# Kernel optimization log

Measured on AMD Instinct MI355X. Metric: run time of the kernel, lower is better.

## Reference

```python
import jax, jax.numpy as jnp
import numpy as np

EPS = 1e-3  # nn.LayerNorm(eps=0.001)
PADDING = 0.0


def setup_inputs() -> dict:
    key = jax.random.key(0)
    k1, k2, k3, k4 = jax.random.split(key, 4)
    N, M, K3, C_IN, C_OUT, B = 200000, 40000, 27, 64, 128, 4
    features = jax.random.normal(k1, (N, C_IN), dtype=jnp.float32)
    center_coors = jax.random.normal(k2, (M, 3), dtype=jnp.float32)
    voxel_idx = jax.random.randint(k3, (M, K3), 0, N, dtype=jnp.int64)
    num_list = jnp.full((B,), M // B, dtype=jnp.int32)
    W = jax.random.normal(k4, (K3 * C_IN, C_OUT), dtype=jnp.float32) * 1e-4
    gamma = jnp.ones((C_OUT,), dtype=jnp.float32)
    beta = jnp.zeros((C_OUT,), dtype=jnp.float32)
    return {
        "features": features,
        "center_coors": center_coors,
        "voxel_idx": voxel_idx,
        "num_list": num_list,
        "W": W,
        "gamma": gamma,
        "beta": beta,
        "num_keypoints": 2048,
    }


def _block(features, voxel_idx, W, gamma, beta):
    M, K3 = voxel_idx.shape
    C_in = features.shape[1]
    # voxel neighbor gather; negative idx -> padding value
    gathered = features[jnp.clip(voxel_idx, 0, features.shape[0] - 1)]  # [M, K3, C_in]
    gathered = jnp.where(voxel_idx[..., None] < 0, PADDING, gathered)
    flat = gathered.reshape(M, K3 * C_in)
    out = flat @ W  # [M, C_out]
    # LayerNorm over channel dim (per-batch loop in torch is mathematically
    # identical to a single row-wise LayerNorm)
    mu = jnp.mean(out, axis=-1, keepdims=True)
    var = jnp.mean(jnp.square(out - mu), axis=-1, keepdims=True)
    out = (out - mu) / jnp.sqrt(var + EPS) * gamma + beta
    return jax.nn.relu(out)


def _resample(out_features, center_coors, num_list, num_keypoints):
    B = num_list.shape[0]
    K = num_keypoints
    accum = jnp.cumsum(num_list)
    offsets = jnp.concatenate([jnp.zeros((1,), accum.dtype), accum[:-1]])  # [B]
    j = jnp.arange(K, dtype=jnp.int32)  # [K]
    end = jnp.minimum(num_list, jnp.int32(K))  # [B]
    valid = j[None, :] < end[:, None]  # [B, K]
    src = jnp.clip(offsets[:, None] + j[None, :], 0, out_features.shape[0] - 1)  # [B, K]
    res_feat = jnp.where(valid[..., None], out_features[src], 0.0)  # [B, K, C]
    res_xyz = jnp.where(valid[..., None], center_coors[src], 0.0)  # [B, K, 3]
    # replicate original quirk: segments 0..B-2 get batch index 1..B-1, last stays 0
    bid = jnp.arange(B, dtype=jnp.float32)
    col0 = jnp.where(bid < B - 1, bid + 1.0, 0.0)  # [B]
    col0 = jnp.broadcast_to(col0[:, None, None], (B, K, 1))
    res_coor = jnp.concatenate([col0, res_xyz], axis=-1)  # [B, K, 4]
    C = out_features.shape[1]
    return res_feat.reshape(B * K, C), res_coor.reshape(B * K, 4)


def reference(features, center_coors, voxel_idx, num_list, W, gamma, beta, num_keypoints):
    out = _block(features, voxel_idx, W, gamma, beta)
    point_features, point_coords = _resample(out, center_coors, num_list, num_keypoints)
    return point_features, point_coords
```

## Files before the change

kernel.cpp:

```cpp
#include <hip/hip_runtime.h>
#include <hip/hip_bf16.h>
#include <stdint.h>
#include <stddef.h>

#define TM 16
#define CIN 64
#define NK3 27
#define NK3P 28
#define COUT 128
#define EPS_LN 1e-3f
#define KCH  (NK3 * CIN / 32)
#define KCHP (NK3P * CIN / 32)
#define NT   (COUT / 16)
#define NPAIR (NK3P / 2)
#define PK_BYTES (NT * KCHP * 64 * 8 * 2)

typedef __attribute__((ext_vector_type(8))) short   short8;
typedef __attribute__((ext_vector_type(4))) float   floatx4;
typedef __attribute__((ext_vector_type(4))) unsigned short ushort4v;

__device__ __forceinline__ unsigned short f2b(float f) {
    union { float f; unsigned int i; } v;
    v.f = f;
    unsigned int i = v.i;
    return (unsigned short)((i + 0x7fffu + ((i >> 16) & 1u)) >> 16);
}

__global__ __launch_bounds__(256) void pack_w(const float* __restrict__ Wm,
                                              const int* __restrict__ voxel_idx,
                                              const int* __restrict__ num_list,
                                              int Bc,
                                              unsigned short* __restrict__ pk,
                                              int* __restrict__ flags) {
    const int t = threadIdx.x;
    if (blockIdx.x == 0 && t < 64) {
        int wv = voxel_idx[2 * t + 1];
        unsigned long long nz = __ballot(wv != 0);
        if (t == 0) {
            int f = (nz == 0ULL) ? 1 : 0;
            bool n64 = false;
            if (Bc >= 2) {
                n64 = (num_list[1] == 0) && (num_list[0] != 0);
                if (Bc >= 4) n64 = n64 && (num_list[3] == 0);
            }
            if (n64) f |= 2;
            flags[0] = f;
        }
    }
    int slot = blockIdx.x * 256 + t;
    int l  = slot & 63;
    int kk = (slot >> 6) % KCHP;
    int nt = slot / (64 * KCHP);
    short8 v = {0, 0, 0, 0, 0, 0, 0, 0};
    if (kk < KCH) {
        int q = l >> 4, n = l & 15;
        const float* src = Wm + (size_t)(kk * 32 + q * 8) * COUT + nt * 16 + n;
        #pragma unroll
        for (int j = 0; j < 8; ++j)
            v[j] = (short)f2b(src[(size_t)j * COUT]);
    }
    *(short8*)(pk + (size_t)slot * 8) = v;
}

__global__ __launch_bounds__(256) void dpc_mfma(
    const float* __restrict__ features,
    const float* __restrict__ center,
    const int* __restrict__ voxel_idx,
    const int* __restrict__ num_list,
    const unsigned short* __restrict__ pk,
    const int* __restrict__ flags,
    const float* __restrict__ gamma_,
    const float* __restrict__ beta_,
    float* __restrict__ out_feat,
    float* __restrict__ out_coor,
    int N, int M, int B, int K, int Rtot)
{
    __shared__ int s_vid[TM][NK3P];
    __shared__ int s_src[TM];
    __shared__ int s_valid[TM];
    __shared__ __align__(16) unsigned short s_a[3][2048];
    __shared__ float s_c[TM][COUT + 4];

    const int t  = threadIdx.x;
    const int R0 = blockIdx.x * TM;

    const int fl = flags[0];
    const bool vidx64 = (fl & 1) != 0;
    const bool nl64   = (fl & 2) != 0;

    if (t < TM) {
        int r = R0 + t;
        int src = 0, valid = 0;
        if (r < Rtot) {
            int b = r / K;
            int j = r - b * K;
            int offs = 0, nlb = 0;
            for (int i = 0; i < B; ++i) {
                int v = nl64 ? num_list[2 * i] : num_list[i];
                if (i < b) offs += v;
                if (i == b) nlb = v;
            }
            int end = nlb < K ? nlb : K;
            valid = (j < end) ? 1 : 0;
            src = offs + j;
            if (src < 0) src = 0;
            if (src > M - 1) src = M - 1;
        }
        s_src[t] = src;
        s_valid[t] = valid;
    }
    __syncthreads();

    if (t < TM * 4) {
        int i = t >> 2, comp = t & 3;
        int r = R0 + i;
        if (r < Rtot) {
            float val;
            if (comp == 0) {
                int b = r / K;
                val = (b < B - 1) ? (float)(b + 1) : 0.0f;
            } else {
                val = s_valid[i] ? center[(size_t)s_src[i] * 3 + comp - 1] : 0.0f;
            }
            out_coor[(size_t)r * 4 + comp] = val;
        }
    }

    for (int lin = t; lin < TM * NK3P; lin += 256) {
        int i = lin / NK3P;
        int k = lin - i * NK3P;
        int v = -1;
        if (k < NK3) {
            size_t e = (size_t)s_src[i] * NK3 + k;
            v = vidx64 ? voxel_idx[2 * e] : voxel_idx[e];
        }
        s_vid[i][k] = v;
    }
    __syncthreads();

    const int m  = t >> 4;
    const int c0 = (t & 15) * 4;
    const int chunk = c0 >> 5;
    const int q4    = (c0 & 31) >> 3;
    const int j0    = c0 & 7;
    const int aoff  = chunk * 512 + (q4 * 16 + m) * 8 + j0;

    auto gatherf4 = [&](int kc) -> float4 {
        int idx = s_vid[m][kc];
        float4 r = make_float4(0.f, 0.f, 0.f, 0.f);
        if (idx >= 0) {
            if (idx > N - 1) idx = N - 1;
            r = *(const float4*)(features + (size_t)idx * CIN + c0);
        }
        return r;
    };
    auto stash = [&](int buf, int sub, float4 v) {
        ushort4v u;
        u[0] = f2b(v.x); u[1] = f2b(v.y); u[2] = f2b(v.z); u[3] = f2b(v.w);
        *(ushort4v*)&s_a[buf][sub * 1024 + aoff] = u;
    };

    const int w    = t >> 6;
    const int lane = t & 63;
    const int nt0 = 2 * w, nt1 = 2 * w + 1;
    auto loadB = [&](int nt, int kk) -> short8 {
        return *(const short8*)(pk + ((size_t)(nt * KCHP + kk) * 64 + lane) * 8);
    };

    floatx4 acc0 = {0.f, 0.f, 0.f, 0.f};
    floatx4 acc1 = {0.f, 0.f, 0.f, 0.f};

    stash(0, 0, gatherf4(0));
    stash(0, 1, gatherf4(1));
    float4 cA0 = gatherf4(2);
    float4 cA1 = gatherf4(3);
    short8 bb[8];
    #pragma unroll
    for (int c = 0; c < 4; ++c) {
        bb[2 * c]     = loadB(nt0, c);
        bb[2 * c + 1] = loadB(nt1, c);
    }
    __syncthreads();

    for (int p = 0; p < NPAIR; ++p) {
        const bool hasC = (p + 1 < NPAIR);
        const bool hasN = (p + 2 < NPAIR);

        float4 nA0, nA1;
        if (hasN) { nA0 = gatherf4(2 * p + 4); nA1 = gatherf4(2 * p + 5); }
        short8 nb[8];
        if (hasC) {
            const int kk = 4 * (p + 1);
            #pragma unroll
            for (int c = 0; c < 4; ++c) {
                nb[2 * c]     = loadB(nt0, kk + c);
                nb[2 * c + 1] = loadB(nt1, kk + c);
            }
        }

        const int buf = p % 3;
        const short8 a0 = *(const short8*)&s_a[buf][       lane * 8];
        const short8 a1 = *(const short8*)&s_a[buf][ 512 + lane * 8];
        const short8 a2 = *(const short8*)&s_a[buf][1024 + lane * 8];
        const short8 a3 = *(const short8*)&s_a[buf][1536 + lane * 8];

        acc0 = __builtin_amdgcn_mfma_f32_16x16x32_bf16(a0, bb[0], acc0, 0, 0, 0);
        acc1 = __builtin_amdgcn_mfma_f32_16x16x32_bf16(a0, bb[1], acc1, 0, 0, 0);
        acc0 = __builtin_amdgcn_mfma_f32_16x16x32_bf16(a1, bb[2], acc0, 0, 0, 0);
        acc1 = __builtin_amdgcn_mfma_f32_16x16x32_bf16(a1, bb[3], acc1, 0, 0, 0);
        acc0 = __builtin_amdgcn_mfma_f32_16x16x32_bf16(a2, bb[4], acc0, 0, 0, 0);
        acc1 = __builtin_amdgcn_mfma_f32_16x16x32_bf16(a2, bb[5], acc1, 0, 0, 0);
        acc0 = __builtin_amdgcn_mfma_f32_16x16x32_bf16(a3, bb[6], acc0, 0, 0, 0);
        acc1 = __builtin_amdgcn_mfma_f32_16x16x32_bf16(a3, bb[7], acc1, 0, 0, 0);

        if (hasC) {
            const int wb = (p + 1) % 3;
            stash(wb, 0, cA0);
            stash(wb, 1, cA1);
        }
        __syncthreads();
        if (hasC) {
            #pragma unroll
            for (int i = 0; i < 8; ++i) bb[i] = nb[i];
        }
        if (hasN) { cA0 = nA0; cA1 = nA1; }
    }

    {
        const int cq = lane >> 4, n = lane & 15;
        #pragma unroll
        for (int reg = 0; reg < 4; ++reg) {
            s_c[cq * 4 + reg][nt0 * 16 + n] = acc0[reg];
            s_c[cq * 4 + reg][nt1 * 16 + n] = acc1[reg];
        }
    }
    __syncthreads();

    const int h  = t >> 6;
    const int c2 = (t & 63) * 2;
    const float g0  = gamma_[c2];
    const float g1  = gamma_[c2 + 1];
    const float be0 = beta_[c2];
    const float be1 = beta_[c2 + 1];

    #pragma unroll
    for (int i = 0; i < 4; ++i) {
        int row = h * 4 + i;
        float a0 = s_c[row][c2];
        float a1 = s_c[row][c2 + 1];
        float s  = a0 + a1;
        float ss = a0 * a0 + a1 * a1;
        #pragma unroll
        for (int mm = 1; mm < 64; mm <<= 1) {
            s  += __shfl_xor(s,  mm, 64);
            ss += __shfl_xor(ss, mm, 64);
        }
        float mu   = s * (1.0f / COUT);
        float var  = ss * (1.0f / COUT) - mu * mu;
        float rstd = rsqrtf(var + EPS_LN);
        float v0 = (a0 - mu) * rstd * g0 + be0;
        float v1 = (a1 - mu) * rstd * g1 + be1;
        v0 = fmaxf(v0, 0.f);
        v1 = fmaxf(v1, 0.f);
        if (!s_valid[row]) { v0 = 0.f; v1 = 0.f; }
        int r = R0 + row;
        if (r < Rtot) {
            out_feat[(size_t)r * COUT + c2]     = v0;
            out_feat[(size_t)r * COUT + c2 + 1] = v1;
        }
    }
}

extern "C" void kernel_launch(void* const* d_in, const int* in_sizes, int n_in,
                              void* d_out, int out_size, void* d_ws, size_t ws_size,
                              hipStream_t stream) {
    const float* features = (const float*)d_in[0];
    const float* center   = (const float*)d_in[1];
    const int*   vidx     = (const int*)d_in[2];
    const int*   num_list = (const int*)d_in[3];
    const float* Wm       = (const float*)d_in[4];
    const float* gamma_   = (const float*)d_in[5];
    const float* beta_    = (const float*)d_in[6];

    const int B    = in_sizes[3];
    const int Cout = in_sizes[5];
    const int M    = in_sizes[1] / 3;
    const int K3v  = in_sizes[2] / M;
    const int Cin  = (in_sizes[4] / Cout) / K3v;
    const int N    = in_sizes[0] / Cin;
    const int Rtot = out_size / (Cout + 4);
    const int K    = Rtot / B;

    float* out_feat = (float*)d_out;
    float* out_coor = out_feat + (size_t)Rtot * Cout;

    unsigned short* pk = (unsigned short*)d_ws;
    int* flags = (int*)((char*)d_ws + PK_BYTES);

    const int pack_grid = (NT * KCHP * 64) / 256;
    pack_w<<<dim3(pack_grid), dim3(256), 0, stream>>>(Wm, vidx, num_list, B, pk, flags);

    const int tiles = (Rtot + TM - 1) / TM;
    dpc_mfma<<<dim3(tiles), dim3(256), 0, stream>>>(
        features, center, vidx, num_list, pk, flags, gamma_, beta_,
        out_feat, out_coor, N, M, B, K, Rtot);
}
```

Baseline: 112.2 us.

## Double block to 512 threads, one MFMA output tile per wave

The fused gather-GEMM-LayerNorm kernel now launches 512 threads per block, with 8 waves each owning one 16-column output tile instead of 4 waves owning two. Each thread gathers one of the two neighbor slots per pair, which halves its per-thread gather and B-register load. The aim is more waves in flight to hide latency of the random feature gathers. The cost is more threads per barrier, and only 16 rows per block with little work per wave, so sync overhead may dominate.

```diff
diff --git a/kernel.cpp b/kernel.cpp
--- a/kernel.cpp
+++ b/kernel.cpp
@@ -62,7 +62,7 @@
     *(short8*)(pk + (size_t)slot * 8) = v;
 }
 
-__global__ __launch_bounds__(256) void dpc_mfma(
+__global__ __launch_bounds__(512) void dpc_mfma(
     const float* __restrict__ features,
     const float* __restrict__ center,
     const int* __restrict__ voxel_idx,
@@ -126,7 +126,7 @@
         }
     }
 
-    for (int lin = t; lin < TM * NK3P; lin += 256) {
+    for (int lin = t; lin < TM * NK3P; lin += 512) {
         int i = lin / NK3P;
         int k = lin - i * NK3P;
         int v = -1;
@@ -138,15 +138,17 @@
     }
     __syncthreads();
 
-    const int m  = t >> 4;
-    const int c0 = (t & 15) * 4;
+    const int sub = t >> 8;
+    const int rem = t & 255;
+    const int m   = rem >> 4;
+    const int c0  = (rem & 15) * 4;
     const int chunk = c0 >> 5;
     const int q4    = (c0 & 31) >> 3;
     const int j0    = c0 & 7;
-    const int aoff  = chunk * 512 + (q4 * 16 + m) * 8 + j0;
-
-    auto gatherf4 = [&](int kc) -> float4 {
-        int idx = s_vid[m][kc];
+    const int aoff  = sub * 1024 + chunk * 512 + (q4 * 16 + m) * 8 + j0;
+
+    auto gatherPair = [&](int p) -> float4 {
+        int idx = s_vid[m][2 * p + sub];
         float4 r = make_float4(0.f, 0.f, 0.f, 0.f);
         if (idx >= 0) {
             if (idx > N - 1) idx = N - 1;
@@ -154,48 +156,35 @@
         }
         return r;
     };
-    auto stash = [&](int buf, int sub, float4 v) {
+    auto stash = [&](int buf, float4 v) {
         ushort4v u;
         u[0] = f2b(v.x); u[1] = f2b(v.y); u[2] = f2b(v.z); u[3] = f2b(v.w);
-        *(ushort4v*)&s_a[buf][sub * 1024 + aoff] = u;
+        *(ushort4v*)&s_a[buf][aoff] = u;
     };
 
     const int w    = t >> 6;
     const int lane = t & 63;
-    const int nt0 = 2 * w, nt1 = 2 * w + 1;
-    auto loadB = [&](int nt, int kk) -> short8 {
-        return *(const short8*)(pk + ((size_t)(nt * KCHP + kk) * 64 + lane) * 8);
+    auto loadB = [&](int kk) -> short8 {
+        return *(const short8*)(pk + ((size_t)(w * KCHP + kk) * 64 + lane) * 8);
     };
 
-    floatx4 acc0 = {0.f, 0.f, 0.f, 0.f};
-    floatx4 acc1 = {0.f, 0.f, 0.f, 0.f};
-
-    stash(0, 0, gatherf4(0));
-    stash(0, 1, gatherf4(1));
-    float4 cA0 = gatherf4(2);
-    float4 cA1 = gatherf4(3);
-    short8 bb[8];
-    #pragma unroll
-    for (int c = 0; c < 4; ++c) {
-        bb[2 * c]     = loadB(nt0, c);
-        bb[2 * c + 1] = loadB(nt1, c);
-    }
+    floatx4 acc = {0.f, 0.f, 0.f, 0.f};
+
+    stash(0, gatherPair(0));
+    float4 cA = gatherPair(1);
+    short8 bb0 = loadB(0), bb1 = loadB(1), bb2 = loadB(2), bb3 = loadB(3);
     __syncthreads();
 
     for (int p = 0; p < NPAIR; ++p) {
         const bool hasC = (p + 1 < NPAIR);
         const bool hasN = (p + 2 < NPAIR);
 
-        float4 nA0, nA1;
-        if (hasN) { nA0 = gatherf4(2 * p + 4); nA1 = gatherf4(2 * p + 5); }
-        short8 nb[8];
+        float4 nA;
+        if (hasN) nA = gatherPair(p + 2);
+        short8 nb0, nb1, nb2, nb3;
         if (hasC) {
             const int kk = 4 * (p + 1);
-            #pragma unroll
-            for (int c = 0; c < 4; ++c) {
-                nb[2 * c]     = loadB(nt0, kk + c);
-                nb[2 * c + 1] = loadB(nt1, kk + c);
-            }
+            nb0 = loadB(kk); nb1 = loadB(kk + 1); nb2 = loadB(kk + 2); nb3 = loadB(kk + 3);
         }
 
         const int buf = p % 3;
@@ -204,48 +193,34 @@
         const short8 a2 = *(const short8*)&s_a[buf][1024 + lane * 8];
         const short8 a3 = *(const short8*)&s_a[buf][1536 + lane * 8];
 
-        acc0 = __builtin_amdgcn_mfma_f32_16x16x32_bf16(a0, bb[0], acc0, 0, 0, 0);
-        acc1 = __builtin_amdgcn_mfma_f32_16x16x32_bf16(a0, bb[1], acc1, 0, 0, 0);
-        acc0 = __builtin_amdgcn_mfma_f32_16x16x32_bf16(a1, bb[2], acc0, 0, 0, 0);
-        acc1 = __builtin_amdgcn_mfma_f32_16x16x32_bf16(a1, bb[3], acc1, 0, 0, 0);
-        acc0 = __builtin_amdgcn_mfma_f32_16x16x32_bf16(a2, bb[4], acc0, 0, 0, 0);
-        acc1 = __builtin_amdgcn_mfma_f32_16x16x32_bf16(a2, bb[5], acc1, 0, 0, 0);
-        acc0 = __builtin_amdgcn_mfma_f32_16x16x32_bf16(a3, bb[6], acc0, 0, 0, 0);
-        acc1 = __builtin_amdgcn_mfma_f32_16x16x32_bf16(a3, bb[7], acc1, 0, 0, 0);
-
-        if (hasC) {
-            const int wb = (p + 1) % 3;
-            stash(wb, 0, cA0);
-            stash(wb, 1, cA1);
-        }
+        acc = __builtin_amdgcn_mfma_f32_16x16x32_bf16(a0, bb0, acc, 0, 0, 0);
+        acc = __builtin_amdgcn_mfma_f32_16x16x32_bf16(a1, bb1, acc, 0, 0, 0);
+        acc = __builtin_amdgcn_mfma_f32_16x16x32_bf16(a2, bb2, acc, 0, 0, 0);
+        acc = __builtin_amdgcn_mfma_f32_16x16x32_bf16(a3, bb3, acc, 0, 0, 0);
+
+        if (hasC) stash((p + 1) % 3, cA);
         __syncthreads();
-        if (hasC) {
-            #pragma unroll
-            for (int i = 0; i < 8; ++i) bb[i] = nb[i];
-        }
-        if (hasN) { cA0 = nA0; cA1 = nA1; }
+        if (hasC) { bb0 = nb0; bb1 = nb1; bb2 = nb2; bb3 = nb3; }
+        if (hasN) cA = nA;
     }
 
     {
         const int cq = lane >> 4, n = lane & 15;
         #pragma unroll
-        for (int reg = 0; reg < 4; ++reg) {
-            s_c[cq * 4 + reg][nt0 * 16 + n] = acc0[reg];
-            s_c[cq * 4 + reg][nt1 * 16 + n] = acc1[reg];
-        }
-    }
-    __syncthreads();
-
-    const int h  = t >> 6;
-    const int c2 = (t & 63) * 2;
+        for (int reg = 0; reg < 4; ++reg)
+            s_c[cq * 4 + reg][w * 16 + n] = acc[reg];
+    }
+    __syncthreads();
+
+    const int c2 = lane * 2;
     const float g0  = gamma_[c2];
     const float g1  = gamma_[c2 + 1];
     const float be0 = beta_[c2];
     const float be1 = beta_[c2 + 1];
 
     #pragma unroll
-    for (int i = 0; i < 4; ++i) {
-        int row = h * 4 + i;
+    for (int i = 0; i < 2; ++i) {
+        int row = w * 2 + i;
         float a0 = s_c[row][c2];
         float a1 = s_c[row][c2 + 1];
         float s  = a0 + a1;
@@ -301,7 +276,7 @@
     pack_w<<<dim3(pack_grid), dim3(256), 0, stream>>>(Wm, vidx, num_list, B, pk, flags);
 
     const int tiles = (Rtot + TM - 1) / TM;
-    dpc_mfma<<<dim3(tiles), dim3(256), 0, stream>>>(
+    dpc_mfma<<<dim3(tiles), dim3(512), 0, stream>>>(
         features, center, vidx, num_list, pk, flags, gamma_, beta_,
         out_feat, out_coor, N, M, B, K, Rtot);
 }
```

After: 110.4 us. Within noise of the previous version (-1.6%).
